# Kernel tuning notes

Measured on AMD Instinct MI355X. Metric: run time of the kernel, lower is better.

## Reference

```python
import jax, jax.numpy as jnp
import numpy as np

IN_C = 128
KEY_C = 128
VAL_C = 128
HEADS = 8
N_CLS = 4

def setup_inputs() -> dict:
    key = jax.random.key(0)
    ks = jax.random.split(key, 10)
    n, c, d, h, w = 2, IN_C, 16, 64, 64
    x = jax.random.normal(ks[0], (n, c, d, h, w), dtype=jnp.float32)
    CLS = jax.random.normal(ks[1], (n, KEY_C, N_CLS), dtype=jnp.float32)
    s = 0.02
    Wk = jax.random.normal(ks[2], (KEY_C, IN_C), dtype=jnp.float32) * s
    bk = jnp.zeros((KEY_C,), dtype=jnp.float32)
    Wq = jax.random.normal(ks[3], (KEY_C, IN_C), dtype=jnp.float32) * s
    bq = jnp.zeros((KEY_C,), dtype=jnp.float32)
    Wv = jax.random.normal(ks[4], (VAL_C, IN_C), dtype=jnp.float32) * s
    bv = jnp.zeros((VAL_C,), dtype=jnp.float32)
    Wr = jax.random.normal(ks[5], (IN_C, VAL_C), dtype=jnp.float32) * s
    br = jnp.zeros((IN_C,), dtype=jnp.float32)
    return {"x": x, "CLS": CLS, "Wk": Wk, "bk": bk, "Wq": Wq, "bq": bq,
            "Wv": Wv, "bv": bv, "Wr": Wr, "br": br}

def reference(x, CLS, Wk, bk, Wq, bq, Wv, bv, Wr, br):
    n, c, d, h, w = x.shape
    L = d * h * w
    xf = x.reshape(n, c, L)
    # 1x1 Conv3d == channel matmul
    keys = jnp.einsum('oc,ncl->nol', Wk, xf) + bk[None, :, None]
    queries = jnp.einsum('oc,ncl->nol', Wq, xf) + bq[None, :, None]
    values = jnp.einsum('oc,ncl->nol', Wv, xf) + bv[None, :, None]
    # prepend CLS tokens along the sequence axis
    keys = jnp.concatenate([CLS, keys], axis=-1)      # (n, kc, L+4)
    queries = jnp.concatenate([CLS, queries], axis=-1)
    values = jnp.concatenate([CLS, values], axis=-1)
    Lt = L + N_CLS
    hk = KEY_C // HEADS
    hv = VAL_C // HEADS
    # contiguous channel slices per head == reshape (n, HEADS, hk, Lt)
    k = jax.nn.softmax(keys.reshape(n, HEADS, hk, Lt), axis=3)    # softmax over sequence
    q = jax.nn.softmax(queries.reshape(n, HEADS, hk, Lt), axis=2) # softmax over head channels
    v = values.reshape(n, HEADS, hv, Lt)
    context = jnp.einsum('nhkl,nhvl->nhkv', k, v)                 # (n, H, hk, hv)
    att = jnp.einsum('nhkv,nhkl->nhvl', context, q)               # (n, H, hv, Lt)
    # original loop reassigns CLS each head; final value comes from last head
    CLS_out = att[:, -1, :, :N_CLS]                               # (n, hv, 4)
    agg = att[:, :, :, N_CLS:].reshape(n, HEADS * hv, L)          # concat over heads
    attention = (jnp.einsum('oc,ncl->nol', Wr, agg) + br[None, :, None]).reshape(n, c, d, h, w)
    context_last = context[:, -1]                                 # last head's context
    return (attention, context_last, CLS_out)
```

## Files before the change

### kernel.cpp

```cpp
#include <hip/hip_runtime.h>

typedef unsigned short u16;
typedef short bf16x8 __attribute__((ext_vector_type(8)));
typedef float floatx4 __attribute__((ext_vector_type(4)));

#define L_TOT 65536
#define OUT_CTX 16777216
#define OUT_CLS (OUT_CTX + 512)

__device__ __forceinline__ u16 f2b(float f) {
  unsigned int u = __float_as_uint(f);
  u += 0x7fffu + ((u >> 16) & 1u);
  return (u16)(u >> 16);
}
__device__ __forceinline__ float blo(unsigned int u) { return __uint_as_float(u << 16); }
__device__ __forceinline__ float bhi(unsigned int u) { return __uint_as_float(u & 0xffff0000u); }

__device__ __forceinline__ float pack_val(const float* W, int eo) {
  int mt = eo >> 11;
  int rem = eo & 2047;
  int ks = rem >> 9;
  int lane = (rem >> 3) & 63;
  int j = rem & 7;
  int row = mt * 16 + (lane & 15);
  int col = ks * 32 + (lane >> 4) * 8 + j;
  return W[row * 128 + col];
}

__global__ __launch_bounds__(256) void kP(
    const float* __restrict__ Wk, const float* __restrict__ Wq,
    const float* __restrict__ Wv, const float* __restrict__ Wr,
    const float* __restrict__ CLS,
    float* __restrict__ S, float* __restrict__ Cnum,
    u16* __restrict__ wkv, u16* __restrict__ wqf, u16* __restrict__ wrf) {
  const int t = threadIdx.x;
  if (blockIdx.x < 32) {
    #pragma unroll
    for (int i = 0; i < 8; ++i) {
      int e = blockIdx.x * 2048 + i * 256 + t;
      if (e < 32768) {
        wkv[e] = f2b(pack_val(e < 16384 ? Wk : Wv, e & 16383));
      } else if (e < 49152) {
        int eq = e - 32768;
        wqf[eq] = f2b(pack_val(Wq, eq));
      } else {
        int er = e - 49152;
        wrf[er] = f2b(pack_val(Wr, er));
      }
    }
  } else {
    int n = t >> 7, r = t & 127;
    float s = 0.f;
    #pragma unroll
    for (int j = 0; j < 4; ++j) s += __expf(CLS[(n * 128 + r) * 4 + j]);
    S[n * 128 + r] = s;
    for (int i = 0; i < 16; ++i) {
      int o = t * 16 + i;
      int nn = o >> 11;
      int rem = o & 2047;
      int h = rem >> 8;
      int kc = (rem >> 4) & 15;
      int vc = rem & 15;
      float a = 0.f;
      #pragma unroll
      for (int j = 0; j < 4; ++j)
        a += __expf(CLS[(nn * 128 + h * 16 + kc) * 4 + j]) *
             CLS[(nn * 128 + h * 16 + vc) * 4 + j];
      Cnum[o] = a;
    }
  }
}

__global__ __launch_bounds__(256) void kA(
    const float* __restrict__ x, const float* __restrict__ bk,
    const float* __restrict__ bv, float* __restrict__ S,
    float* __restrict__ Cnum, const u16* __restrict__ wkv) {
  __shared__ __align__(16) u16 xT[64][136];
  __shared__ __align__(16) u16 ev[256][72];
  const int t = threadIdx.x;
  const int w = t >> 6, lane = t & 63;
  const int quad = lane >> 4, lm = lane & 15;
  const int n = blockIdx.x >> 8;
  const int l0base = (blockIdx.x & 255) << 8;

  const int sc = t >> 4;
  const int sl4 = t & 15;

  float4 pf[8];
  #pragma unroll
  for (int i = 0; i < 8; ++i) {
    int c = i * 16 + sc;
    pf[i] = *(const float4*)(x + (((size_t)(n * 128 + c)) << 16) + l0base + sl4 * 4);
  }

  bf16x8 wf[4][4];
  #pragma unroll
  for (int mt = 0; mt < 4; ++mt) {
    int rb = (mt < 2) ? (2 * w + mt) : (8 + 2 * w + (mt - 2));
    #pragma unroll
    for (int ks = 0; ks < 4; ++ks)
      wf[mt][ks] = *(const bf16x8*)(wkv + (((rb * 4 + ks) * 64 + lane) * 8));
  }
  float bias_[4][4];
  #pragma unroll
  for (int mt = 0; mt < 4; ++mt)
    #pragma unroll
    for (int j = 0; j < 4; ++j) {
      int r = w * 32 + (mt & 1) * 16 + quad * 4 + j;
      bias_[mt][j] = (mt < 2) ? bk[r] : bv[r];
    }

  floatx4 z4 = {0.f, 0.f, 0.f, 0.f};
  floatx4 cacc[2] = {z4, z4};
  float sacc = 0.f;

  for (int tile = 0; tile < 4; ++tile) {
    {
      int c = sc;
      #pragma unroll
      for (int i = 0; i < 8; ++i) {
        int cc = i * 16 + sc;
        int col = sl4 * 4;
        xT[col + 0][cc] = f2b(pf[i].x);
        xT[col + 1][cc] = f2b(pf[i].y);
        xT[col + 2][cc] = f2b(pf[i].z);
        xT[col + 3][cc] = f2b(pf[i].w);
      }
      (void)c;
    }
    __syncthreads();

    floatx4 acc[4][4];
    #pragma unroll
    for (int mt = 0; mt < 4; ++mt)
      #pragma unroll
      for (int nt = 0; nt < 4; ++nt) acc[mt][nt] = z4;

    #pragma unroll
    for (int nt = 0; nt < 4; ++nt)
      #pragma unroll
      for (int ks = 0; ks < 4; ++ks) {
        bf16x8 b = *(const bf16x8*)(&xT[nt * 16 + lm][ks * 32 + quad * 8]);
        #pragma unroll
        for (int mt = 0; mt < 4; ++mt)
          acc[mt][nt] = __builtin_amdgcn_mfma_f32_16x16x32_bf16(wf[mt][ks], b, acc[mt][nt], 0, 0, 0);
      }

    #pragma unroll
    for (int mt = 0; mt < 4; ++mt)
      #pragma unroll
      for (int j = 0; j < 4; ++j) {
        int R = ((mt < 2) ? 0 : 128) + w * 32 + (mt & 1) * 16 + quad * 4 + j;
        #pragma unroll
        for (int nt = 0; nt < 4; ++nt) {
          float v = acc[mt][nt][j] + bias_[mt][j];
          if (mt < 2) v = __expf(v);
          ev[R][nt * 16 + lm] = f2b(v);
        }
      }

    if (tile < 3) {
      int l0 = l0base + (tile + 1) * 64;
      #pragma unroll
      for (int i = 0; i < 8; ++i) {
        int c = i * 16 + sc;
        pf[i] = *(const float4*)(x + (((size_t)(n * 128 + c)) << 16) + l0 + sl4 * 4);
      }
    }
    __syncthreads();

    #pragma unroll
    for (int hh = 0; hh < 2; ++hh) {
      int h = w * 2 + hh;
      #pragma unroll
      for (int ks = 0; ks < 2; ++ks) {
        bf16x8 aE = *(const bf16x8*)(&ev[h * 16 + lm][ks * 32 + quad * 8]);
        bf16x8 bV = *(const bf16x8*)(&ev[128 + h * 16 + lm][ks * 32 + quad * 8]);
        cacc[hh] = __builtin_amdgcn_mfma_f32_16x16x32_bf16(aE, bV, cacc[hh], 0, 0, 0);
      }
    }
    if (t < 128) {
      #pragma unroll
      for (int i = 0; i < 8; ++i) {
        uint4 u = *(const uint4*)(&ev[t][i * 8]);
        sacc += blo(u.x) + bhi(u.x) + blo(u.y) + bhi(u.y) +
                blo(u.z) + bhi(u.z) + blo(u.w) + bhi(u.w);
      }
    }
  }

  #pragma unroll
  for (int hh = 0; hh < 2; ++hh) {
    int h = w * 2 + hh;
    #pragma unroll
    for (int j = 0; j < 4; ++j)
      atomicAdd(&Cnum[((n * 8 + h) * 16 + quad * 4 + j) * 16 + lm], cacc[hh][j]);
  }
  if (t < 128) atomicAdd(&S[n * 128 + t], sacc);
}

__global__ __launch_bounds__(256) void kF(
    const float* __restrict__ CLS, const float* __restrict__ S,
    const float* __restrict__ Cnum, u16* __restrict__ ctxf,
    float* __restrict__ out) {
  const int t = threadIdx.x;
  for (int e = t; e < 8192; e += 256) {
    int n = e >> 12;
    int rem = e & 4095;
    int h = rem >> 9;
    int rem2 = rem & 511;
    int lane = rem2 >> 3;
    int j = rem2 & 7;
    int m = lane & 15;
    int k = (lane >> 4) * 8 + j;
    float v = 0.f;
    if (k < 16) v = Cnum[((n * 8 + h) * 16 + k) * 16 + m] / S[n * 128 + h * 16 + k];
    ctxf[e] = f2b(v);
  }
  for (int e = t; e < 512; e += 256) {
    int n = e >> 8;
    int kc = (e >> 4) & 15;
    int vc = e & 15;
    out[OUT_CTX + e] = Cnum[((n * 8 + 7) * 16 + kc) * 16 + vc] / S[n * 128 + 112 + kc];
  }
  if (t < 128) {
    int n = t >> 6;
    int vc = (t >> 2) & 15;
    int j = t & 3;
    float den = 0.f, num = 0.f;
    #pragma unroll
    for (int kc = 0; kc < 16; ++kc) {
      float e_ = __expf(CLS[(n * 128 + 112 + kc) * 4 + j]);
      den += e_;
      num += e_ * (Cnum[((n * 8 + 7) * 16 + kc) * 16 + vc] / S[n * 128 + 112 + kc]);
    }
    out[OUT_CLS + t] = num / den;
  }
}

__global__ __launch_bounds__(256) void kB(
    const float* __restrict__ x, const float* __restrict__ bq,
    const float* __restrict__ br, const u16* __restrict__ wqf,
    const u16* __restrict__ wrf, const u16* __restrict__ ctxf,
    float* __restrict__ out) {
  __shared__ __align__(16) u16 xT[64][136];
  __shared__ __align__(16) u16 qT[64][136];
  __shared__ __align__(16) u16 aT[64][136];
  const int t = threadIdx.x;
  const int w = t >> 6, lane = t & 63;
  const int quad = lane >> 4, lm = lane & 15;
  const int n = blockIdx.x >> 8;
  const int l0base = (blockIdx.x & 255) << 8;

  const int sc = t >> 4;
  const int sl4 = t & 15;

  float4 pf[8];
  #pragma unroll
  for (int i = 0; i < 8; ++i) {
    int c = i * 16 + sc;
    pf[i] = *(const float4*)(x + (((size_t)(n * 128 + c)) << 16) + l0base + sl4 * 4);
  }

  bf16x8 wq[2][4], wr[2][4];
  #pragma unroll
  for (int mt = 0; mt < 2; ++mt)
    #pragma unroll
    for (int ks = 0; ks < 4; ++ks) {
      wq[mt][ks] = *(const bf16x8*)(wqf + ((((w * 2 + mt) * 4 + ks) * 64 + lane) * 8));
      wr[mt][ks] = *(const bf16x8*)(wrf + ((((w * 2 + mt) * 4 + ks) * 64 + lane) * 8));
    }
  bf16x8 aC[2];
  #pragma unroll
  for (int mt = 0; mt < 2; ++mt)
    aC[mt] = *(const bf16x8*)(ctxf + (((size_t)(n * 8 + w * 2 + mt)) * 64 + lane) * 8);

  float bqv_[2][4], brv[2][4];
  #pragma unroll
  for (int mt = 0; mt < 2; ++mt)
    #pragma unroll
    for (int j = 0; j < 4; ++j) {
      bqv_[mt][j] = bq[(w * 2 + mt) * 16 + quad * 4 + j];
      brv[mt][j] = br[(w * 2 + mt) * 16 + quad * 4 + j];
    }

  floatx4 z4 = {0.f, 0.f, 0.f, 0.f};

  for (int tile = 0; tile < 4; ++tile) {
    int l0 = l0base + tile * 64;
    #pragma unroll
    for (int i = 0; i < 8; ++i) {
      int cc = i * 16 + sc;
      int col = sl4 * 4;
      xT[col + 0][cc] = f2b(pf[i].x);
      xT[col + 1][cc] = f2b(pf[i].y);
      xT[col + 2][cc] = f2b(pf[i].z);
      xT[col + 3][cc] = f2b(pf[i].w);
    }
    __syncthreads();

    floatx4 acc[2][4];
    #pragma unroll
    for (int mt = 0; mt < 2; ++mt)
      #pragma unroll
      for (int nt = 0; nt < 4; ++nt) acc[mt][nt] = z4;

    #pragma unroll
    for (int nt = 0; nt < 4; ++nt)
      #pragma unroll
      for (int ks = 0; ks < 4; ++ks) {
        bf16x8 b = *(const bf16x8*)(&xT[nt * 16 + lm][ks * 32 + quad * 8]);
        #pragma unroll
        for (int mt = 0; mt < 2; ++mt)
          acc[mt][nt] = __builtin_amdgcn_mfma_f32_16x16x32_bf16(wq[mt][ks], b, acc[mt][nt], 0, 0, 0);
      }

    #pragma unroll
    for (int mt = 0; mt < 2; ++mt) {
      int h = w * 2 + mt;
      #pragma unroll
      for (int nt = 0; nt < 4; ++nt) {
        float e[4];
        float ssum = 0.f;
        #pragma unroll
        for (int j = 0; j < 4; ++j) {
          e[j] = __expf(acc[mt][nt][j] + bqv_[mt][j]);
          ssum += e[j];
        }
        ssum += __shfl_xor(ssum, 16);
        ssum += __shfl_xor(ssum, 32);
        float inv = 1.f / ssum;
        #pragma unroll
        for (int j = 0; j < 4; ++j)
          qT[nt * 16 + lm][h * 16 + quad * 4 + j] = f2b(e[j] * inv);
      }
    }

    #pragma unroll
    for (int mt = 0; mt < 2; ++mt) {
      int h = w * 2 + mt;
      #pragma unroll
      for (int nt = 0; nt < 4; ++nt) {
        bf16x8 bq_ = *(const bf16x8*)(&qT[nt * 16 + lm][h * 16 + (quad & 1) * 8]);
        floatx4 d = __builtin_amdgcn_mfma_f32_16x16x32_bf16(aC[mt], bq_, z4, 0, 0, 0);
        #pragma unroll
        for (int j = 0; j < 4; ++j)
          aT[nt * 16 + lm][h * 16 + quad * 4 + j] = f2b(d[j]);
      }
    }

    if (tile < 3) {
      int l0n = l0base + (tile + 1) * 64;
      #pragma unroll
      for (int i = 0; i < 8; ++i) {
        int c = i * 16 + sc;
        pf[i] = *(const float4*)(x + (((size_t)(n * 128 + c)) << 16) + l0n + sl4 * 4);
      }
    }
    __syncthreads();

    floatx4 acc2[2][4];
    #pragma unroll
    for (int mt = 0; mt < 2; ++mt)
      #pragma unroll
      for (int nt = 0; nt < 4; ++nt) acc2[mt][nt] = z4;

    #pragma unroll
    for (int nt = 0; nt < 4; ++nt)
      #pragma unroll
      for (int ks = 0; ks < 4; ++ks) {
        bf16x8 b = *(const bf16x8*)(&aT[nt * 16 + lm][ks * 32 + quad * 8]);
        #pragma unroll
        for (int mt = 0; mt < 2; ++mt)
          acc2[mt][nt] = __builtin_amdgcn_mfma_f32_16x16x32_bf16(wr[mt][ks], b, acc2[mt][nt], 0, 0, 0);
      }

    #pragma unroll
    for (int mt = 0; mt < 2; ++mt)
      #pragma unroll
      for (int j = 0; j < 4; ++j) {
        int R = (w * 2 + mt) * 16 + quad * 4 + j;
        #pragma unroll
        for (int nt = 0; nt < 4; ++nt)
          out[(((size_t)(n * 128 + R)) << 16) + l0 + nt * 16 + lm] = acc2[mt][nt][j] + brv[mt][j];
      }
  }
}

extern "C" void kernel_launch(void* const* d_in, const int* in_sizes, int n_in,
                              void* d_out, int out_size, void* d_ws, size_t ws_size,
                              hipStream_t stream) {
  const float* x   = (const float*)d_in[0];
  const float* CLS = (const float*)d_in[1];
  const float* Wk  = (const float*)d_in[2];
  const float* bk  = (const float*)d_in[3];
  const float* Wq  = (const float*)d_in[4];
  const float* bq  = (const float*)d_in[5];
  const float* Wv  = (const float*)d_in[6];
  const float* bv  = (const float*)d_in[7];
  const float* Wr  = (const float*)d_in[8];
  const float* br  = (const float*)d_in[9];
  float* out = (float*)d_out;
  char* ws = (char*)d_ws;
  float* S    = (float*)(ws + 0);
  float* Cnum = (float*)(ws + 1024);
  u16* ctxf   = (u16*)(ws + 17408);
  u16* wkv    = (u16*)(ws + 33792);
  u16* wqf    = (u16*)(ws + 99328);
  u16* wrf    = (u16*)(ws + 132096);

  kP<<<33, 256, 0, stream>>>(Wk, Wq, Wv, Wr, CLS, S, Cnum, wkv, wqf, wrf);
  kA<<<512, 256, 0, stream>>>(x, bk, bv, S, Cnum, wkv);
  kF<<<1, 256, 0, stream>>>(CLS, S, Cnum, ctxf, out);
  kB<<<512, 256, 0, stream>>>(x, bq, br, wqf, wrf, ctxf, out);
}
```

Measured before the change: 176.4 us.

## Fold finalize kernel into kB, double grid, split atomic slots, stream weights

Removes the single-block kF finalize kernel. Each kB block now rebuilds its normalized context fragment from Cnum/S, and block 0 writes the context and CLS outputs. kA and kB launch 1024 blocks of 128 columns instead of 512 of 256, with launch bounds set to 3 blocks per SM. Atomics go to two alternating slots to reduce contention. Weight fragments are now double-buffered per k-step from global memory rather than held in registers, and the second half of the x channels is loaded synchronously inside the tile, which may expose load latency.

```diff
diff --git a/kernel.cpp b/kernel.cpp
--- a/kernel.cpp
+++ b/kernel.cpp
@@ -31,7 +31,7 @@
     const float* __restrict__ Wk, const float* __restrict__ Wq,
     const float* __restrict__ Wv, const float* __restrict__ Wr,
     const float* __restrict__ CLS,
-    float* __restrict__ S, float* __restrict__ Cnum,
+    float* __restrict__ S2, float* __restrict__ Cnum2,
     u16* __restrict__ wkv, u16* __restrict__ wqf, u16* __restrict__ wrf) {
   const int t = threadIdx.x;
   if (blockIdx.x < 32) {
@@ -53,7 +53,8 @@
     float s = 0.f;
     #pragma unroll
     for (int j = 0; j < 4; ++j) s += __expf(CLS[(n * 128 + r) * 4 + j]);
-    S[n * 128 + r] = s;
+    S2[n * 128 + r] = s;
+    S2[256 + n * 128 + r] = 0.f;
     for (int i = 0; i < 16; ++i) {
       int o = t * 16 + i;
       int nn = o >> 11;
@@ -66,41 +67,35 @@
       for (int j = 0; j < 4; ++j)
         a += __expf(CLS[(nn * 128 + h * 16 + kc) * 4 + j]) *
              CLS[(nn * 128 + h * 16 + vc) * 4 + j];
-      Cnum[o] = a;
-    }
-  }
-}
-
-__global__ __launch_bounds__(256) void kA(
+      Cnum2[o] = a;
+      Cnum2[4096 + o] = 0.f;
+    }
+  }
+}
+
+__global__ __launch_bounds__(256, 3) void kA(
     const float* __restrict__ x, const float* __restrict__ bk,
-    const float* __restrict__ bv, float* __restrict__ S,
-    float* __restrict__ Cnum, const u16* __restrict__ wkv) {
+    const float* __restrict__ bv, float* __restrict__ S2,
+    float* __restrict__ Cnum2, const u16* __restrict__ wkv) {
   __shared__ __align__(16) u16 xT[64][136];
   __shared__ __align__(16) u16 ev[256][72];
   const int t = threadIdx.x;
   const int w = t >> 6, lane = t & 63;
   const int quad = lane >> 4, lm = lane & 15;
-  const int n = blockIdx.x >> 8;
-  const int l0base = (blockIdx.x & 255) << 8;
+  const int n = blockIdx.x >> 9;
+  const int l0base = (blockIdx.x & 511) << 7;
+  const int slot = blockIdx.x & 1;
 
   const int sc = t >> 4;
   const int sl4 = t & 15;
 
-  float4 pf[8];
-  #pragma unroll
-  for (int i = 0; i < 8; ++i) {
+  float4 pf[4];
+  #pragma unroll
+  for (int i = 0; i < 4; ++i) {
     int c = i * 16 + sc;
     pf[i] = *(const float4*)(x + (((size_t)(n * 128 + c)) << 16) + l0base + sl4 * 4);
   }
 
-  bf16x8 wf[4][4];
-  #pragma unroll
-  for (int mt = 0; mt < 4; ++mt) {
-    int rb = (mt < 2) ? (2 * w + mt) : (8 + 2 * w + (mt - 2));
-    #pragma unroll
-    for (int ks = 0; ks < 4; ++ks)
-      wf[mt][ks] = *(const bf16x8*)(wkv + (((rb * 4 + ks) * 64 + lane) * 8));
-  }
   float bias_[4][4];
   #pragma unroll
   for (int mt = 0; mt < 4; ++mt)
@@ -114,19 +109,33 @@
   floatx4 cacc[2] = {z4, z4};
   float sacc = 0.f;
 
-  for (int tile = 0; tile < 4; ++tile) {
+  for (int tile = 0; tile < 2; ++tile) {
+    #pragma unroll
+    for (int i = 0; i < 4; ++i) {
+      int cc = i * 16 + sc;
+      int col = sl4 * 4;
+      xT[col + 0][cc] = f2b(pf[i].x);
+      xT[col + 1][cc] = f2b(pf[i].y);
+      xT[col + 2][cc] = f2b(pf[i].z);
+      xT[col + 3][cc] = f2b(pf[i].w);
+    }
     {
-      int c = sc;
-      #pragma unroll
-      for (int i = 0; i < 8; ++i) {
-        int cc = i * 16 + sc;
+      int l0 = l0base + tile * 64;
+      float4 v2[4];
+      #pragma unroll
+      for (int i = 0; i < 4; ++i) {
+        int c = (i + 4) * 16 + sc;
+        v2[i] = *(const float4*)(x + (((size_t)(n * 128 + c)) << 16) + l0 + sl4 * 4);
+      }
+      #pragma unroll
+      for (int i = 0; i < 4; ++i) {
+        int cc = (i + 4) * 16 + sc;
         int col = sl4 * 4;
-        xT[col + 0][cc] = f2b(pf[i].x);
-        xT[col + 1][cc] = f2b(pf[i].y);
-        xT[col + 2][cc] = f2b(pf[i].z);
-        xT[col + 3][cc] = f2b(pf[i].w);
-      }
-      (void)c;
+        xT[col + 0][cc] = f2b(v2[i].x);
+        xT[col + 1][cc] = f2b(v2[i].y);
+        xT[col + 2][cc] = f2b(v2[i].z);
+        xT[col + 3][cc] = f2b(v2[i].w);
+      }
     }
     __syncthreads();
 
@@ -136,15 +145,30 @@
       #pragma unroll
       for (int nt = 0; nt < 4; ++nt) acc[mt][nt] = z4;
 
-    #pragma unroll
-    for (int nt = 0; nt < 4; ++nt)
-      #pragma unroll
-      for (int ks = 0; ks < 4; ++ks) {
+    bf16x8 wfk[2][4];
+    #pragma unroll
+    for (int mt = 0; mt < 4; ++mt) {
+      int rb = (mt < 2) ? (2 * w + mt) : (8 + 2 * w + (mt - 2));
+      wfk[0][mt] = *(const bf16x8*)(wkv + (((rb * 4 + 0) * 64 + lane) * 8));
+    }
+    #pragma unroll
+    for (int ks = 0; ks < 4; ++ks) {
+      int cur = ks & 1;
+      if (ks < 3) {
+        #pragma unroll
+        for (int mt = 0; mt < 4; ++mt) {
+          int rb = (mt < 2) ? (2 * w + mt) : (8 + 2 * w + (mt - 2));
+          wfk[cur ^ 1][mt] = *(const bf16x8*)(wkv + (((rb * 4 + ks + 1) * 64 + lane) * 8));
+        }
+      }
+      #pragma unroll
+      for (int nt = 0; nt < 4; ++nt) {
         bf16x8 b = *(const bf16x8*)(&xT[nt * 16 + lm][ks * 32 + quad * 8]);
         #pragma unroll
         for (int mt = 0; mt < 4; ++mt)
-          acc[mt][nt] = __builtin_amdgcn_mfma_f32_16x16x32_bf16(wf[mt][ks], b, acc[mt][nt], 0, 0, 0);
-      }
+          acc[mt][nt] = __builtin_amdgcn_mfma_f32_16x16x32_bf16(wfk[cur][mt], b, acc[mt][nt], 0, 0, 0);
+      }
+    }
 
     #pragma unroll
     for (int mt = 0; mt < 4; ++mt)
@@ -159,10 +183,10 @@
         }
       }
 
-    if (tile < 3) {
-      int l0 = l0base + (tile + 1) * 64;
-      #pragma unroll
-      for (int i = 0; i < 8; ++i) {
+    if (tile < 1) {
+      int l0 = l0base + 64;
+      #pragma unroll
+      for (int i = 0; i < 4; ++i) {
         int c = i * 16 + sc;
         pf[i] = *(const float4*)(x + (((size_t)(n * 128 + c)) << 16) + l0 + sl4 * 4);
       }
@@ -189,59 +213,22 @@
     }
   }
 
+  float* Cn = Cnum2 + slot * 4096;
   #pragma unroll
   for (int hh = 0; hh < 2; ++hh) {
     int h = w * 2 + hh;
     #pragma unroll
     for (int j = 0; j < 4; ++j)
-      atomicAdd(&Cnum[((n * 8 + h) * 16 + quad * 4 + j) * 16 + lm], cacc[hh][j]);
-  }
-  if (t < 128) atomicAdd(&S[n * 128 + t], sacc);
-}
-
-__global__ __launch_bounds__(256) void kF(
-    const float* __restrict__ CLS, const float* __restrict__ S,
-    const float* __restrict__ Cnum, u16* __restrict__ ctxf,
-    float* __restrict__ out) {
-  const int t = threadIdx.x;
-  for (int e = t; e < 8192; e += 256) {
-    int n = e >> 12;
-    int rem = e & 4095;
-    int h = rem >> 9;
-    int rem2 = rem & 511;
-    int lane = rem2 >> 3;
-    int j = rem2 & 7;
-    int m = lane & 15;
-    int k = (lane >> 4) * 8 + j;
-    float v = 0.f;
-    if (k < 16) v = Cnum[((n * 8 + h) * 16 + k) * 16 + m] / S[n * 128 + h * 16 + k];
-    ctxf[e] = f2b(v);
-  }
-  for (int e = t; e < 512; e += 256) {
-    int n = e >> 8;
-    int kc = (e >> 4) & 15;
-    int vc = e & 15;
-    out[OUT_CTX + e] = Cnum[((n * 8 + 7) * 16 + kc) * 16 + vc] / S[n * 128 + 112 + kc];
-  }
-  if (t < 128) {
-    int n = t >> 6;
-    int vc = (t >> 2) & 15;
-    int j = t & 3;
-    float den = 0.f, num = 0.f;
-    #pragma unroll
-    for (int kc = 0; kc < 16; ++kc) {
-      float e_ = __expf(CLS[(n * 128 + 112 + kc) * 4 + j]);
-      den += e_;
-      num += e_ * (Cnum[((n * 8 + 7) * 16 + kc) * 16 + vc] / S[n * 128 + 112 + kc]);
-    }
-    out[OUT_CLS + t] = num / den;
-  }
-}
-
-__global__ __launch_bounds__(256) void kB(
+      atomicAdd(&Cn[((n * 8 + h) * 16 + quad * 4 + j) * 16 + lm], cacc[hh][j]);
+  }
+  if (t < 128) atomicAdd(&S2[slot * 256 + n * 128 + t], sacc);
+}
+
+__global__ __launch_bounds__(256, 3) void kB(
     const float* __restrict__ x, const float* __restrict__ bq,
     const float* __restrict__ br, const u16* __restrict__ wqf,
-    const u16* __restrict__ wrf, const u16* __restrict__ ctxf,
+    const u16* __restrict__ wrf, const float* __restrict__ S2,
+    const float* __restrict__ Cnum2, const float* __restrict__ CLS,
     float* __restrict__ out) {
   __shared__ __align__(16) u16 xT[64][136];
   __shared__ __align__(16) u16 qT[64][136];
@@ -249,31 +236,66 @@
   const int t = threadIdx.x;
   const int w = t >> 6, lane = t & 63;
   const int quad = lane >> 4, lm = lane & 15;
-  const int n = blockIdx.x >> 8;
-  const int l0base = (blockIdx.x & 255) << 8;
+  const int n = blockIdx.x >> 9;
+  const int l0base = (blockIdx.x & 511) << 7;
 
   const int sc = t >> 4;
   const int sl4 = t & 15;
 
-  float4 pf[8];
-  #pragma unroll
-  for (int i = 0; i < 8; ++i) {
+  float4 pf[4];
+  #pragma unroll
+  for (int i = 0; i < 4; ++i) {
     int c = i * 16 + sc;
     pf[i] = *(const float4*)(x + (((size_t)(n * 128 + c)) << 16) + l0base + sl4 * 4);
   }
 
-  bf16x8 wq[2][4], wr[2][4];
-  #pragma unroll
-  for (int mt = 0; mt < 2; ++mt)
-    #pragma unroll
-    for (int ks = 0; ks < 4; ++ks) {
-      wq[mt][ks] = *(const bf16x8*)(wqf + ((((w * 2 + mt) * 4 + ks) * 64 + lane) * 8));
-      wr[mt][ks] = *(const bf16x8*)(wrf + ((((w * 2 + mt) * 4 + ks) * 64 + lane) * 8));
-    }
   bf16x8 aC[2];
   #pragma unroll
-  for (int mt = 0; mt < 2; ++mt)
-    aC[mt] = *(const bf16x8*)(ctxf + (((size_t)(n * 8 + w * 2 + mt)) * 64 + lane) * 8);
+  for (int mt = 0; mt < 2; ++mt) {
+    int h = w * 2 + mt;
+    short frag[8];
+    #pragma unroll
+    for (int j = 0; j < 8; ++j) {
+      int k = quad * 8 + j;
+      float v = 0.f;
+      if (k < 16) {
+        int ci = ((n * 8 + h) * 16 + k) * 16 + lm;
+        float c = Cnum2[ci] + Cnum2[4096 + ci];
+        float s = S2[n * 128 + h * 16 + k] + S2[256 + n * 128 + h * 16 + k];
+        v = c / s;
+      }
+      frag[j] = (short)f2b(v);
+    }
+    aC[mt] = *(bf16x8*)frag;
+  }
+
+  if (blockIdx.x == 0) {
+    for (int e = t; e < 512; e += 256) {
+      int nn = e >> 8;
+      int kc = (e >> 4) & 15;
+      int vc = e & 15;
+      int ci = ((nn * 8 + 7) * 16 + kc) * 16 + vc;
+      float c = Cnum2[ci] + Cnum2[4096 + ci];
+      float s = S2[nn * 128 + 112 + kc] + S2[256 + nn * 128 + 112 + kc];
+      out[OUT_CTX + e] = c / s;
+    }
+    if (t < 128) {
+      int nn = t >> 6;
+      int vc = (t >> 2) & 15;
+      int j = t & 3;
+      float den = 0.f, num = 0.f;
+      #pragma unroll
+      for (int kc = 0; kc < 16; ++kc) {
+        float e_ = __expf(CLS[(nn * 128 + 112 + kc) * 4 + j]);
+        int ci = ((nn * 8 + 7) * 16 + kc) * 16 + vc;
+        float c = Cnum2[ci] + Cnum2[4096 + ci];
+        float s = S2[nn * 128 + 112 + kc] + S2[256 + nn * 128 + 112 + kc];
+        den += e_;
+        num += e_ * (c / s);
+      }
+      out[OUT_CLS + t] = num / den;
+    }
+  }
 
   float bqv_[2][4], brv[2][4];
   #pragma unroll
@@ -286,10 +308,10 @@
 
   floatx4 z4 = {0.f, 0.f, 0.f, 0.f};
 
-  for (int tile = 0; tile < 4; ++tile) {
+  for (int tile = 0; tile < 2; ++tile) {
     int l0 = l0base + tile * 64;
     #pragma unroll
-    for (int i = 0; i < 8; ++i) {
+    for (int i = 0; i < 4; ++i) {
       int cc = i * 16 + sc;
       int col = sl4 * 4;
       xT[col + 0][cc] = f2b(pf[i].x);
@@ -297,6 +319,23 @@
       xT[col + 2][cc] = f2b(pf[i].z);
       xT[col + 3][cc] = f2b(pf[i].w);
     }
+    {
+      float4 v2[4];
+      #pragma unroll
+      for (int i = 0; i < 4; ++i) {
+        int c = (i + 4) * 16 + sc;
+        v2[i] = *(const float4*)(x + (((size_t)(n * 128 + c)) << 16) + l0 + sl4 * 4);
+      }
+      #pragma unroll
+      for (int i = 0; i < 4; ++i) {
+        int cc = (i + 4) * 16 + sc;
+        int col = sl4 * 4;
+        xT[col + 0][cc] = f2b(v2[i].x);
+        xT[col + 1][cc] = f2b(v2[i].y);
+        xT[col + 2][cc] = f2b(v2[i].z);
+        xT[col + 3][cc] = f2b(v2[i].w);
+      }
+    }
     __syncthreads();
 
     floatx4 acc[2][4];
@@ -305,15 +344,26 @@
       #pragma unroll
       for (int nt = 0; nt < 4; ++nt) acc[mt][nt] = z4;
 
-    #pragma unroll
-    for (int nt = 0; nt < 4; ++nt)
-      #pragma unroll
-      for (int ks = 0; ks < 4; ++ks) {
+    bf16x8 wqk[2][2];
+    #pragma unroll
+    for (int mt = 0; mt < 2; ++mt)
+      wqk[0][mt] = *(const bf16x8*)(wqf + ((((w * 2 + mt) * 4 + 0) * 64 + lane) * 8));
+    #pragma unroll
+    for (int ks = 0; ks < 4; ++ks) {
+      int cur = ks & 1;
+      if (ks < 3) {
+        #pragma unroll
+        for (int mt = 0; mt < 2; ++mt)
+          wqk[cur ^ 1][mt] = *(const bf16x8*)(wqf + ((((w * 2 + mt) * 4 + ks + 1) * 64 + lane) * 8));
+      }
+      #pragma unroll
+      for (int nt = 0; nt < 4; ++nt) {
         bf16x8 b = *(const bf16x8*)(&xT[nt * 16 + lm][ks * 32 + quad * 8]);
         #pragma unroll
         for (int mt = 0; mt < 2; ++mt)
-          acc[mt][nt] = __builtin_amdgcn_mfma_f32_16x16x32_bf16(wq[mt][ks], b, acc[mt][nt], 0, 0, 0);
-      }
+          acc[mt][nt] = __builtin_amdgcn_mfma_f32_16x16x32_bf16(wqk[cur][mt], b, acc[mt][nt], 0, 0, 0);
+      }
+    }
 
     #pragma unroll
     for (int mt = 0; mt < 2; ++mt) {
@@ -349,10 +399,10 @@
       }
     }
 
-    if (tile < 3) {
-      int l0n = l0base + (tile + 1) * 64;
-      #pragma unroll
-      for (int i = 0; i < 8; ++i) {
+    if (tile < 1) {
+      int l0n = l0base + 64;
+      #pragma unroll
+      for (int i = 0; i < 4; ++i) {
         int c = i * 16 + sc;
         pf[i] = *(const float4*)(x + (((size_t)(n * 128 + c)) << 16) + l0n + sl4 * 4);
       }
@@ -365,15 +415,26 @@
       #pragma unroll
       for (int nt = 0; nt < 4; ++nt) acc2[mt][nt] = z4;
 
-    #pragma unroll
-    for (int nt = 0; nt < 4; ++nt)
-      #pragma unroll
-      for (int ks = 0; ks < 4; ++ks) {
+    bf16x8 wrk[2][2];
+    #pragma unroll
+    for (int mt = 0; mt < 2; ++mt)
+      wrk[0][mt] = *(const bf16x8*)(wrf + ((((w * 2 + mt) * 4 + 0) * 64 + lane) * 8));
+    #pragma unroll
+    for (int ks = 0; ks < 4; ++ks) {
+      int cur = ks & 1;
+      if (ks < 3) {
+        #pragma unroll
+        for (int mt = 0; mt < 2; ++mt)
+          wrk[cur ^ 1][mt] = *(const bf16x8*)(wrf + ((((w * 2 + mt) * 4 + ks + 1) * 64 + lane) * 8));
+      }
+      #pragma unroll
+      for (int nt = 0; nt < 4; ++nt) {
         bf16x8 b = *(const bf16x8*)(&aT[nt * 16 + lm][ks * 32 + quad * 8]);
         #pragma unroll
         for (int mt = 0; mt < 2; ++mt)
-          acc2[mt][nt] = __builtin_amdgcn_mfma_f32_16x16x32_bf16(wr[mt][ks], b, acc2[mt][nt], 0, 0, 0);
-      }
+          acc2[mt][nt] = __builtin_amdgcn_mfma_f32_16x16x32_bf16(wrk[cur][mt], b, acc2[mt][nt], 0, 0, 0);
+      }
+    }
 
     #pragma unroll
     for (int mt = 0; mt < 2; ++mt)
@@ -402,15 +463,13 @@
   const float* br  = (const float*)d_in[9];
   float* out = (float*)d_out;
   char* ws = (char*)d_ws;
-  float* S    = (float*)(ws + 0);
-  float* Cnum = (float*)(ws + 1024);
-  u16* ctxf   = (u16*)(ws + 17408);
-  u16* wkv    = (u16*)(ws + 33792);
-  u16* wqf    = (u16*)(ws + 99328);
-  u16* wrf    = (u16*)(ws + 132096);
-
-  kP<<<33, 256, 0, stream>>>(Wk, Wq, Wv, Wr, CLS, S, Cnum, wkv, wqf, wrf);
-  kA<<<512, 256, 0, stream>>>(x, bk, bv, S, Cnum, wkv);
-  kF<<<1, 256, 0, stream>>>(CLS, S, Cnum, ctxf, out);
-  kB<<<512, 256, 0, stream>>>(x, bq, br, wqf, wrf, ctxf, out);
-}
+  float* S2    = (float*)(ws + 0);
+  float* Cnum2 = (float*)(ws + 2048);
+  u16* wkv     = (u16*)(ws + 34816);
+  u16* wqf     = (u16*)(ws + 100352);
+  u16* wrf     = (u16*)(ws + 133120);
+
+  kP<<<33, 256, 0, stream>>>(Wk, Wq, Wv, Wr, CLS, S2, Cnum2, wkv, wqf, wrf);
+  kA<<<1024, 256, 0, stream>>>(x, bk, bv, S2, Cnum2, wkv);
+  kB<<<1024, 256, 0, stream>>>(x, bq, br, wqf, wrf, S2, Cnum2, CLS, out);
+}
```

After: 244.1 us. 38.4% more time.

## Fold finalize kernel into kB and split atomic accumulators into two slots

Applied to the files above, without the earlier changes.

Removes the single-block kF launch by having every kB block compute its own context fragment directly from the accumulated numerators and denominators. Block 0 of kB also writes the context and CLS outputs. The atomic accumulators in kA are split into two slots by block parity, which halves contention on each address, and kB sums the two slots. The cost is that every kB block redundantly does a few scalar divides and global reads, in exchange for one fewer serial launch and one fewer dependency bubble.

```diff
diff --git a/kernel.cpp b/kernel.cpp
--- a/kernel.cpp
+++ b/kernel.cpp
@@ -31,7 +31,7 @@
     const float* __restrict__ Wk, const float* __restrict__ Wq,
     const float* __restrict__ Wv, const float* __restrict__ Wr,
     const float* __restrict__ CLS,
-    float* __restrict__ S, float* __restrict__ Cnum,
+    float* __restrict__ S2, float* __restrict__ Cnum2,
     u16* __restrict__ wkv, u16* __restrict__ wqf, u16* __restrict__ wrf) {
   const int t = threadIdx.x;
   if (blockIdx.x < 32) {
@@ -53,7 +53,8 @@
     float s = 0.f;
     #pragma unroll
     for (int j = 0; j < 4; ++j) s += __expf(CLS[(n * 128 + r) * 4 + j]);
-    S[n * 128 + r] = s;
+    S2[n * 128 + r] = s;
+    S2[256 + n * 128 + r] = 0.f;
     for (int i = 0; i < 16; ++i) {
       int o = t * 16 + i;
       int nn = o >> 11;
@@ -66,15 +67,16 @@
       for (int j = 0; j < 4; ++j)
         a += __expf(CLS[(nn * 128 + h * 16 + kc) * 4 + j]) *
              CLS[(nn * 128 + h * 16 + vc) * 4 + j];
-      Cnum[o] = a;
+      Cnum2[o] = a;
+      Cnum2[4096 + o] = 0.f;
     }
   }
 }
 
 __global__ __launch_bounds__(256) void kA(
     const float* __restrict__ x, const float* __restrict__ bk,
-    const float* __restrict__ bv, float* __restrict__ S,
-    float* __restrict__ Cnum, const u16* __restrict__ wkv) {
+    const float* __restrict__ bv, float* __restrict__ S2,
+    float* __restrict__ Cnum2, const u16* __restrict__ wkv) {
   __shared__ __align__(16) u16 xT[64][136];
   __shared__ __align__(16) u16 ev[256][72];
   const int t = threadIdx.x;
@@ -82,6 +84,7 @@
   const int quad = lane >> 4, lm = lane & 15;
   const int n = blockIdx.x >> 8;
   const int l0base = (blockIdx.x & 255) << 8;
+  const int slot = blockIdx.x & 1;
 
   const int sc = t >> 4;
   const int sl4 = t & 15;
@@ -115,18 +118,14 @@
   float sacc = 0.f;
 
   for (int tile = 0; tile < 4; ++tile) {
-    {
-      int c = sc;
-      #pragma unroll
-      for (int i = 0; i < 8; ++i) {
-        int cc = i * 16 + sc;
-        int col = sl4 * 4;
-        xT[col + 0][cc] = f2b(pf[i].x);
-        xT[col + 1][cc] = f2b(pf[i].y);
-        xT[col + 2][cc] = f2b(pf[i].z);
-        xT[col + 3][cc] = f2b(pf[i].w);
-      }
-      (void)c;
+    #pragma unroll
+    for (int i = 0; i < 8; ++i) {
+      int cc = i * 16 + sc;
+      int col = sl4 * 4;
+      xT[col + 0][cc] = f2b(pf[i].x);
+      xT[col + 1][cc] = f2b(pf[i].y);
+      xT[col + 2][cc] = f2b(pf[i].z);
+      xT[col + 3][cc] = f2b(pf[i].w);
     }
     __syncthreads();
 
@@ -189,59 +188,22 @@
     }
   }
 
+  float* Cn = Cnum2 + slot * 4096;
   #pragma unroll
   for (int hh = 0; hh < 2; ++hh) {
     int h = w * 2 + hh;
     #pragma unroll
     for (int j = 0; j < 4; ++j)
-      atomicAdd(&Cnum[((n * 8 + h) * 16 + quad * 4 + j) * 16 + lm], cacc[hh][j]);
-  }
-  if (t < 128) atomicAdd(&S[n * 128 + t], sacc);
-}
-
-__global__ __launch_bounds__(256) void kF(
-    const float* __restrict__ CLS, const float* __restrict__ S,
-    const float* __restrict__ Cnum, u16* __restrict__ ctxf,
-    float* __restrict__ out) {
-  const int t = threadIdx.x;
-  for (int e = t; e < 8192; e += 256) {
-    int n = e >> 12;
-    int rem = e & 4095;
-    int h = rem >> 9;
-    int rem2 = rem & 511;
-    int lane = rem2 >> 3;
-    int j = rem2 & 7;
-    int m = lane & 15;
-    int k = (lane >> 4) * 8 + j;
-    float v = 0.f;
-    if (k < 16) v = Cnum[((n * 8 + h) * 16 + k) * 16 + m] / S[n * 128 + h * 16 + k];
-    ctxf[e] = f2b(v);
-  }
-  for (int e = t; e < 512; e += 256) {
-    int n = e >> 8;
-    int kc = (e >> 4) & 15;
-    int vc = e & 15;
-    out[OUT_CTX + e] = Cnum[((n * 8 + 7) * 16 + kc) * 16 + vc] / S[n * 128 + 112 + kc];
-  }
-  if (t < 128) {
-    int n = t >> 6;
-    int vc = (t >> 2) & 15;
-    int j = t & 3;
-    float den = 0.f, num = 0.f;
-    #pragma unroll
-    for (int kc = 0; kc < 16; ++kc) {
-      float e_ = __expf(CLS[(n * 128 + 112 + kc) * 4 + j]);
-      den += e_;
-      num += e_ * (Cnum[((n * 8 + 7) * 16 + kc) * 16 + vc] / S[n * 128 + 112 + kc]);
-    }
-    out[OUT_CLS + t] = num / den;
-  }
+      atomicAdd(&Cn[((n * 8 + h) * 16 + quad * 4 + j) * 16 + lm], cacc[hh][j]);
+  }
+  if (t < 128) atomicAdd(&S2[slot * 256 + n * 128 + t], sacc);
 }
 
 __global__ __launch_bounds__(256) void kB(
     const float* __restrict__ x, const float* __restrict__ bq,
     const float* __restrict__ br, const u16* __restrict__ wqf,
-    const u16* __restrict__ wrf, const u16* __restrict__ ctxf,
+    const u16* __restrict__ wrf, const float* __restrict__ S2,
+    const float* __restrict__ Cnum2, const float* __restrict__ CLS,
     float* __restrict__ out) {
   __shared__ __align__(16) u16 xT[64][136];
   __shared__ __align__(16) u16 qT[64][136];
@@ -270,10 +232,54 @@
       wq[mt][ks] = *(const bf16x8*)(wqf + ((((w * 2 + mt) * 4 + ks) * 64 + lane) * 8));
       wr[mt][ks] = *(const bf16x8*)(wrf + ((((w * 2 + mt) * 4 + ks) * 64 + lane) * 8));
     }
+
   bf16x8 aC[2];
   #pragma unroll
-  for (int mt = 0; mt < 2; ++mt)
-    aC[mt] = *(const bf16x8*)(ctxf + (((size_t)(n * 8 + w * 2 + mt)) * 64 + lane) * 8);
+  for (int mt = 0; mt < 2; ++mt) {
+    int h = w * 2 + mt;
+    short frag[8];
+    #pragma unroll
+    for (int j = 0; j < 8; ++j) {
+      int k = quad * 8 + j;
+      float v = 0.f;
+      if (k < 16) {
+        int ci = ((n * 8 + h) * 16 + k) * 16 + lm;
+        float c = Cnum2[ci] + Cnum2[4096 + ci];
+        float s = S2[n * 128 + h * 16 + k] + S2[256 + n * 128 + h * 16 + k];
+        v = c / s;
+      }
+      frag[j] = (short)f2b(v);
+    }
+    aC[mt] = *(bf16x8*)frag;
+  }
+
+  if (blockIdx.x == 0) {
+    for (int e = t; e < 512; e += 256) {
+      int nn = e >> 8;
+      int kc = (e >> 4) & 15;
+      int vc = e & 15;
+      int ci = ((nn * 8 + 7) * 16 + kc) * 16 + vc;
+      float c = Cnum2[ci] + Cnum2[4096 + ci];
+      float s = S2[nn * 128 + 112 + kc] + S2[256 + nn * 128 + 112 + kc];
+      out[OUT_CTX + e] = c / s;
+    }
+    if (t < 128) {
+      int nn = t >> 6;
+      int vc = (t >> 2) & 15;
+      int j = t & 3;
+      float den = 0.f, num = 0.f;
+      #pragma unroll
+      for (int kc = 0; kc < 16; ++kc) {
+        float e_ = __expf(CLS[(nn * 128 + 112 + kc) * 4 + j]);
+        int ci = ((nn * 8 + 7) * 16 + kc) * 16 + vc;
+        float c = Cnum2[ci] + Cnum2[4096 + ci];
+        float s = S2[nn * 128 + 112 + kc] + S2[256 + nn * 128 + 112 + kc];
+        den += e_;
+        num += e_ * (c / s);
+      }
+      out[OUT_CLS + t] = num / den;
+    }
+  }
 
   float bqv_[2][4], brv[2][4];
   #pragma unroll
@@ -402,15 +408,13 @@
   const float* br  = (const float*)d_in[9];
   float* out = (float*)d_out;
   char* ws = (char*)d_ws;
-  float* S    = (float*)(ws + 0);
-  float* Cnum = (float*)(ws + 1024);
-  u16* ctxf   = (u16*)(ws + 17408);
-  u16* wkv    = (u16*)(ws + 33792);
-  u16* wqf    = (u16*)(ws + 99328);
-  u16* wrf    = (u16*)(ws + 132096);
-
-  kP<<<33, 256, 0, stream>>>(Wk, Wq, Wv, Wr, CLS, S, Cnum, wkv, wqf, wrf);
-  kA<<<512, 256, 0, stream>>>(x, bk, bv, S, Cnum, wkv);
-  kF<<<1, 256, 0, stream>>>(CLS, S, Cnum, ctxf, out);
-  kB<<<512, 256, 0, stream>>>(x, bq, br, wqf, wrf, ctxf, out);
-}
+  float* S2    = (float*)(ws + 0);
+  float* Cnum2 = (float*)(ws + 2048);
+  u16* wkv     = (u16*)(ws + 34816);
+  u16* wqf     = (u16*)(ws + 100352);
+  u16* wrf     = (u16*)(ws + 133120);
+
+  kP<<<33, 256, 0, stream>>>(Wk, Wq, Wv, Wr, CLS, S2, Cnum2, wkv, wqf, wrf);
+  kA<<<512, 256, 0, stream>>>(x, bk, bv, S2, Cnum2, wkv);
+  kB<<<512, 256, 0, stream>>>(x, bq, br, wqf, wrf, S2, Cnum2, CLS, out);
+}
```

Result: faster. 167.9 us (-4.8%).
